# Optimization experiments

Hardware: AMD Instinct MI355X
Metric: run time of the kernel (lower is better)

The kernel has to match this reference:

```python
import jax, jax.numpy as jnp
import numpy as np

V_A, V_HP = 256, 256
H_A, H_HP = 2048, 4096
DEPTH = 12


def lstm_cell(x, h, c, W_ih, W_hh, b_ih, b_hh):
    # PyTorch LSTM cell: gate order i, f, g, o along the 4H axis.
    gates = x @ W_ih.T + h @ W_hh.T + (b_ih + b_hh)
    i, f, g, o = jnp.split(gates, 4, axis=-1)
    c_new = jax.nn.sigmoid(f) * c + jax.nn.sigmoid(i) * jnp.tanh(g)
    h_new = jax.nn.sigmoid(o) * jnp.tanh(c_new)
    return h_new, c_new


def setup_inputs() -> dict:
    key = jax.random.key(0)
    ks = jax.random.split(key, 16)
    s = jnp.float32(0.02)
    f32 = jnp.float32
    return {
        "x_thought_vec_arch": jax.random.normal(ks[0], (1, 1, H_A), f32),
        "x_thought_vec_arch_hp": jax.random.normal(ks[1], (1, 1, H_HP), f32),
        # arch LSTM (input V_A, hidden H_A)
        "W_ih_a": jax.random.normal(ks[2], (4 * H_A, V_A), f32) * s,
        "W_hh_a": jax.random.normal(ks[3], (4 * H_A, H_A), f32) * s,
        "b_ih_a": jax.random.normal(ks[4], (4 * H_A,), f32) * s,
        "b_hh_a": jax.random.normal(ks[5], (4 * H_A,), f32) * s,
        # arch_out Linear (H_A -> V_A)
        "W_out_a": jax.random.normal(ks[6], (V_A, H_A), f32) * s,
        "b_out_a": jax.random.normal(ks[7], (V_A,), f32) * s,
        # hp_summarizer Linear (H_HP -> H_HP//2)
        "W_sum": jax.random.normal(ks[8], (H_HP // 2, H_HP), f32) * s,
        "b_sum": jax.random.normal(ks[9], (H_HP // 2,), f32) * s,
        # arch_hp LSTM (input V_A + V_HP, hidden H_HP)
        "W_ih_hp": jax.random.normal(ks[10], (4 * H_HP, V_A + V_HP), f32) * s,
        "W_hh_hp": jax.random.normal(ks[11], (4 * H_HP, H_HP), f32) * s,
        "b_ih_hp": jax.random.normal(ks[12], (4 * H_HP,), f32) * s,
        "b_hh_hp": jax.random.normal(ks[13], (4 * H_HP,), f32) * s,
        # arch_hp_out Linear (H_HP -> V_HP)
        "W_out_hp": jax.random.normal(ks[14], (V_HP, H_HP), f32) * s,
        "b_out_hp": jax.random.normal(ks[15], (V_HP,), f32) * s,
    }


def reference(x_thought_vec_arch, x_thought_vec_arch_hp,
              W_ih_a, W_hh_a, b_ih_a, b_hh_a, W_out_a, b_out_a,
              W_sum, b_sum, W_ih_hp, W_hh_hp, b_ih_hp, b_hh_hp,
              W_out_hp, b_out_hp):
    h_a, h_hp = x_thought_vec_arch, x_thought_vec_arch_hp  # thought vecs used as hidden states
    c_a = jnp.zeros_like(h_a)
    c_hp = jnp.zeros_like(h_hp)
    a = jnp.full((1, 1, V_A), 1.0 / V_A, jnp.float32)       # SOS soft one-hot
    a_hp = jnp.full((1, 1, V_HP), 1.0 / V_HP, jnp.float32)

    def step(carry, _):
        a, a_hp, h_a, c_a, h_hp, c_hp = carry
        # forward_arch: seq_len=1 so LSTM output == new hidden
        h_a, c_a = lstm_cell(a, h_a, c_a, W_ih_a, W_hh_a, b_ih_a, b_hh_a)
        a = jax.nn.softmax(h_a @ W_out_a.T + b_out_a, axis=-1)
        # forward_arch_hp (keeps the original's swapped hx=(c_hp, prev_h_hp)):
        h_sum = jax.nn.relu(h_hp @ W_sum.T + b_sum)
        prev_h_hp = jnp.concatenate([h_a, h_sum], axis=-1)   # used as CELL state
        inp = jnp.concatenate([a, a_hp], axis=-1)
        h_hp, c_hp = lstm_cell(inp, c_hp, prev_h_hp, W_ih_hp, W_hh_hp, b_ih_hp, b_hh_hp)
        a_hp = jax.nn.softmax(h_hp @ W_out_hp.T + b_out_hp, axis=-1)
        return (a, a_hp, h_a, c_a, h_hp, c_hp), (a, a_hp)

    _, (ys_a, ys_hp) = jax.lax.scan(step, (a, a_hp, h_a, c_a, h_hp, c_hp), None, length=DEPTH)
    # torch.cat(list_of_(1,1,V), dim=1) -> (1, DEPTH, V)
    arch = ys_a.reshape(DEPTH, V_A)[None]
    arch_hp = ys_hp.reshape(DEPTH, V_HP)[None]
    return arch, arch_hp
```

## Files before the change

### kernel.cpp

```cpp
#include <hip/hip_runtime.h>
#include <hip/hip_fp16.h>
#include <hip/hip_cooperative_groups.h>

namespace cg = cooperative_groups;

#define H_A   2048
#define H_HP  4096
#define DEPTH 12

struct Half8 { __half2 a, b, c, d; };
struct Half4 { __half2 a, b; };

__device__ __forceinline__ float fsig_(float x) { return 1.0f / (1.0f + __expf(-x)); }
__device__ __forceinline__ float ftanh_(float x) {
    return 1.0f - 2.0f / (__expf(2.0f * x) + 1.0f);
}
__device__ __forceinline__ float dot4_(float4 a, float4 b) {
    return a.x * b.x + a.y * b.y + a.z * b.z + a.w * b.w;
}
__device__ __forceinline__ float dot8h_(Half8 w, float4 x0, float4 x1) {
    float2 wa = __half22float2(w.a), wb = __half22float2(w.b);
    float2 wc = __half22float2(w.c), wd = __half22float2(w.d);
    return wa.x * x0.x + wa.y * x0.y + wb.x * x0.z + wb.y * x0.w +
           wc.x * x1.x + wc.y * x1.y + wd.x * x1.z + wd.y * x1.w;
// ... 25 lines not shown
        a2 += __shfl_xor(a2, off, 64);
        a3 += __shfl_xor(a3, off, 64);
    }
}

struct Params {
    const float *x_a, *x_hp;
    const float *W_ih_a, *W_hh_a, *b_ih_a, *b_hh_a;
    const float *W_out_a, *b_out_a, *W_sum, *b_sum;
    const float *W_ih_hp, *W_hh_hp, *b_ih_hp, *b_hh_hp, *W_out_hp, *b_out_hp;
    __half *hW_ih_a, *hW_hh_a, *hW_sum, *hW_ih_hp, *hW_hh_hp, *hW_out_a, *hW_out_hp;
    float *gates_a, *h_sum, *gacc, *h_a, *c_a0, *c_a1, *h_hp, *c_hp;
    float *logits_a, *logits_hp, *a_vec, *out;
};

__global__ __launch_bounds__(256) void decoder_persistent(Params p)
{
    cg::grid_group grid = cg::this_grid();
    __shared__ float sbuf[2056];
    const int tid = threadIdx.x, lane = tid & 63, wv = tid >> 6;
    const int waveId = (blockIdx.x << 2) | wv;
    const int nw = (gridDim.x << 2);

    for (int t = 0; t < DEPTH; ++t) {
        {
            const int limit = (t == 0) ? 26624 : 26880;
            for (int r = waveId; r < limit; r += nw) {
                if (r < 8192) {
                    float acc;
                    if (t == 0) {
                        float4 wf = ((const float4*)(p.W_ih_a + (size_t)r * 256))[lane];
                        ((Half4*)(p.hW_ih_a + (size_t)r * 256))[lane] = cvt4_(wf);
                        acc = (wf.x + wf.y + wf.z + wf.w) * (1.0f / 256.0f);
                        const float4* whf = (const float4*)(p.W_hh_a + (size_t)r * H_A);
                        const float4* xh = (const float4*)p.x_a;
                        Half4* dsth = (Half4*)(p.hW_hh_a + (size_t)r * H_A);
#pragma unroll
                        for (int it = 0; it < 8; ++it) {
                            int idx = it * 64 + lane;
                            float4 w = whf[idx];
                            dsth[idx] = cvt4_(w);
                            acc += dot4_(w, xh[idx]);
                        }
                    } else {
                        Half4 w = ((const Half4*)(p.hW_ih_a + (size_t)r * 256))[lane];
                        float4 x = ((const float4*)p.a_vec)[lane];
                        float2 w0 = __half22float2(w.a), w1 = __half22float2(w.b);
                        acc = w0.x * x.x + w0.y * x.y + w1.x * x.z + w1.y * x.w;
                        const Half8* wh = (const Half8*)(p.hW_hh_a + (size_t)r * H_A);
                        const float4* xh = (const float4*)p.h_a;
#pragma unroll
                        for (int it = 0; it < 4; ++it) {
                            int idx = it * 64 + lane;
                            acc += dot8h_(wh[idx], xh[2 * idx], xh[2 * idx + 1]);
                        }
                    }
                    acc = waveReduceSum(acc);
                    if (lane == 0) p.gates_a[r] = acc + p.b_ih_a[r] + p.b_hh_a[r];
                } else if (r < 10240) {
                    const int rr = r - 8192;
                    float acc = 0.0f;
                    if (t == 0) {
                        const float4* wf = (const float4*)(p.W_sum + (size_t)rr * H_HP);
                        const float4* xx = (const float4*)p.x_hp;
                        Half4* dsth = (Half4*)(p.hW_sum + (size_t)rr * H_HP);
#pragma unroll
                        for (int it = 0; it < 16; ++it) {
                            int idx = it * 64 + lane;
                            float4 w = wf[idx];
                            dsth[idx] = cvt4_(w);
                            acc += dot4_(w, xx[idx]);
                        }
                    } else {
                        const Half8* ww = (const Half8*)(p.hW_sum + (size_t)rr * H_HP);
                        const float4* xx = (const float4*)p.h_hp;
#pragma unroll
                        for (int it = 0; it < 8; ++it) {
                            int idx = it * 64 + lane;
                            acc += dot8h_(ww[idx], xx[2 * idx], xx[2 * idx + 1]);
                        }
                    }
                    acc = waveReduceSum(acc);
                    if (lane == 0) p.h_sum[rr] = fmaxf(acc + p.b_sum[rr], 0.0f);
                } else if (r < 26624) {
                    const int rg = r - 10240;
                    if (t == 0) {
                        const float4* wf = (const float4*)(p.W_hh_hp + (size_t)rg * H_HP);
                        Half4* dsth = (Half4*)(p.hW_hh_hp + (size_t)rg * H_HP);
#pragma unroll
                        for (int it = 0; it < 16; ++it) {
                            int idx = it * 64 + lane;
                            dsth[idx] = cvt4_(wf[idx]);
                        }
                        if (lane == 0) p.gacc[rg] = p.b_ih_hp[rg] + p.b_hh_hp[rg];
                    } else {
                        const Half8* ww = (const Half8*)(p.hW_hh_hp + (size_t)rg * H_HP);
                        const float4* xx = (const float4*)p.c_hp;
                        float acc = 0.0f;
#pragma unroll
                        for (int it = 0; it < 8; ++it) {
                            int idx = it * 64 + lane;
                            acc += dot8h_(ww[idx], xx[2 * idx], xx[2 * idx + 1]);
                        }
                        acc = waveReduceSum(acc);
                        if (lane == 0) p.gacc[rg] = acc + p.b_ih_hp[rg] + p.b_hh_hp[rg];
                    }
                } else {
                    const int ro = r - 26624;
                    float acc = 0.0f;
                    const float4* xx = (const float4*)p.h_hp;
                    if (t == 1) {
                        const float4* wf = (const float4*)(p.W_out_hp + (size_t)ro * H_HP);
                        Half4* dsth = (Half4*)(p.hW_out_hp + (size_t)ro * H_HP);
#pragma unroll
                        for (int it = 0; it < 16; ++it) {
                            int idx = it * 64 + lane;
                            float4 w = wf[idx];
                            dsth[idx] = cvt4_(w);
                            acc += dot4_(w, xx[idx]);
                        }
                    } else {
                        const Half8* ww = (const Half8*)(p.hW_out_hp + (size_t)ro * H_HP);
#pragma unroll
                        for (int it = 0; it < 8; ++it) {
                            int idx = it * 64 + lane;
                            acc += dot8h_(ww[idx], xx[2 * idx], xx[2 * idx + 1]);
                        }
                    }
                    acc = waveReduceSum(acc);
                    if (lane == 0) p.logits_hp[ro] = acc + p.b_out_hp[ro];
                }
            }
        }
        grid.sync();

        if (blockIdx.x < 16) {
            float* h_s = sbuf;
            const float* cin = (t & 1) ? p.c_a1 : p.c_a0;
            float* cout = (t & 1) ? p.c_a0 : p.c_a1;
#pragma unroll
            for (int k = 0; k < 8; ++k) {
                int e = tid + k * 256;
                float gi = p.gates_a[e], gf = p.gates_a[H_A + e];
                float gg = p.gates_a[2 * H_A + e], go = p.gates_a[3 * H_A + e];
                float ci = (t == 0) ? 0.0f : cin[e];
                float c = fsig_(gf) * ci + fsig_(gi) * ftanh_(gg);
                float h = fsig_(go) * ftanh_(c);
                h_s[e] = h;
                if (blockIdx.x == 0) { cout[e] = c; p.h_a[e] = h; }
            }
            __syncthreads();
            const float4* h4 = (const float4*)h_s;
            int row = (blockIdx.x << 4) | (wv << 2);
            for (int j = 0; j < 4; ++j, ++row) {
                float acc = 0.0f;
                if (t == 0) {
                    const float4* wf = (const float4*)(p.W_out_a + (size_t)row * H_A);
                    Half4* dsth = (Half4*)(p.hW_out_a + (size_t)row * H_A);
#pragma unroll
                    for (int it = 0; it < 8; ++it) {
                        int idx = it * 64 + lane;
                        float4 w = wf[idx];
                        dsth[idx] = cvt4_(w);
                        acc += dot4_(w, h4[idx]);
                    }
                } else {
                    const Half8* ww = (const Half8*)(p.hW_out_a + (size_t)row * H_A);
#pragma unroll
                    for (int it = 0; it < 4; ++it) {
                        int idx = it * 64 + lane;
                        acc += dot8h_(ww[idx], h4[2 * idx], h4[2 * idx + 1]);
                    }
                }
                acc = waveReduceSum(acc);
                if (lane == 0) p.logits_a[row] = acc + p.b_out_a[row];
            }
        }
        grid.sync();

        {
            float* p_all = sbuf;
            float* red   = sbuf + 512;
            float la = p.logits_a[tid];
            float lh = (t == 0) ? 0.0f : p.logits_hp[tid];
            float ma = la, mh = lh;
#pragma unroll
            for (int off = 32; off > 0; off >>= 1) {
                ma = fmaxf(ma, __shfl_xor(ma, off, 64));
                mh = fmaxf(mh, __shfl_xor(mh, off, 64));
            }
            if (lane == 0) { red[wv] = ma; red[4 + wv] = mh; }
            __syncthreads();
            ma = fmaxf(fmaxf(red[0], red[1]), fmaxf(red[2], red[3]));
            mh = fmaxf(fmaxf(red[4], red[5]), fmaxf(red[6], red[7]));
            __syncthreads();
            float ea = __expf(la - ma), eh = __expf(lh - mh);
            float sa = waveReduceSum(ea), sh = waveReduceSum(eh);
            if (lane == 0) { red[wv] = sa; red[4 + wv] = sh; }
            __syncthreads();
            sa = red[0] + red[1] + red[2] + red[3];
            sh = red[4] + red[5] + red[6] + red[7];
            float pa = ea / sa, ph = eh / sh;
            p_all[tid] = pa;
            p_all[256 + tid] = ph;
            if (blockIdx.x == 0) {
                p.a_vec[tid] = pa;
                p.out[(size_t)t * 256 + tid] = pa;
                if (t > 0) p.out[3072 + (size_t)(t - 1) * 256 + tid] = ph;
            }
            __syncthreads();
            float4 xa = ((const float4*)p_all)[2 * lane];
            float4 xb = ((const float4*)p_all)[2 * lane + 1];
            for (int e = waveId; e < H_HP; e += nw) {
                float s0, s1, s2, s3;
                if (t == 0) {
                    auto rowdot_cvt = [&](int r) -> float {
                        const float4* wf = (const float4*)(p.W_ih_hp + (size_t)r * 512);
                        float4 u = wf[2 * lane], v = wf[2 * lane + 1];
                        ((Half8*)(p.hW_ih_hp + (size_t)r * 512))[lane] = cvt8_(u, v);
                        return dot4_(u, xa) + dot4_(v, xb);
                    };
                    s0 = rowdot_cvt(e);
                    s1 = rowdot_cvt(4096 + e);
                    s2 = rowdot_cvt(8192 + e);
                    s3 = rowdot_cvt(12288 + e);
                } else {
                    Half8 w0 = ((const Half8*)(p.hW_ih_hp + (size_t)e * 512))[lane];
                    Half8 w1 = ((const Half8*)(p.hW_ih_hp + (size_t)(4096 + e) * 512))[lane];
                    Half8 w2 = ((const Half8*)(p.hW_ih_hp + (size_t)(8192 + e) * 512))[lane];
                    Half8 w3 = ((const Half8*)(p.hW_ih_hp + (size_t)(12288 + e) * 512))[lane];
                    s0 = dot8h_(w0, xa, xb);
                    s1 = dot8h_(w1, xa, xb);
                    s2 = dot8h_(w2, xa, xb);
                    s3 = dot8h_(w3, xa, xb);
                }
                waveReduce4(s0, s1, s2, s3);
                if (lane == 0) {
                    float gi = s0 + p.gacc[e];
                    float gf = s1 + p.gacc[4096 + e];
                    float gg = s2 + p.gacc[8192 + e];
                    float go = s3 + p.gacc[12288 + e];
                    float prev = (e < H_A) ? p.h_a[e] : p.h_sum[e - H_A];
                    float c = fsig_(gf) * prev + fsig_(gi) * ftanh_(gg);
                    float h = fsig_(go) * ftanh_(c);
                    p.c_hp[e] = c;
                    p.h_hp[e] = h;
                }
            }
        }
        grid.sync();
    }

    if (blockIdx.x < 16) {
        int row = (blockIdx.x << 4) | (wv << 2);
        const float4* xx = (const float4*)p.h_hp;
        for (int j = 0; j < 4; ++j, ++row) {
            const Half8* ww = (const Half8*)(p.hW_out_hp + (size_t)row * H_HP);
            float acc = 0.0f;
#pragma unroll
            for (int it = 0; it < 8; ++it) {
                int idx = it * 64 + lane;
                acc += dot8h_(ww[idx], xx[2 * idx], xx[2 * idx + 1]);
            }
            acc = waveReduceSum(acc);
            if (lane == 0) p.logits_hp[row] = acc + p.b_out_hp[row];
        }
    }
    grid.sync();
    if (blockIdx.x == 0) {
        float* red = sbuf + 512;
        float v = p.logits_hp[tid];
        float m = v;
#pragma unroll
        for (int off = 32; off > 0; off >>= 1) m = fmaxf(m, __shfl_xor(m, off, 64));
        if (lane == 0) red[wv] = m;
        __syncthreads();
        m = fmaxf(fmaxf(red[0], red[1]), fmaxf(red[2], red[3]));
        __syncthreads();
        float e = __expf(v - m);
        float s = waveReduceSum(e);
        if (lane == 0) red[wv] = s;
        __syncthreads();
        s = red[0] + red[1] + red[2] + red[3];
        p.out[3072 + 11 * 256 + tid] = e / s;
    }
}

__global__ void k_init(const float* __restrict__ x_a, const float* __restrict__ x_hp,
                       float* __restrict__ h_a, float* __restrict__ c_a0,
                       float* __restrict__ h_hp, float* __restrict__ c_hp,
                       float* __restrict__ a_vec, float* __restrict__ logits_hp)
{
    int i = blockIdx.x * 256 + threadIdx.x;
    if (i < H_A)  { h_a[i] = x_a[i];  c_a0[i] = 0.0f; }
    if (i < H_HP) { h_hp[i] = x_hp[i]; c_hp[i] = 0.0f; }
    if (i < 256)  { a_vec[i] = 1.0f / 256.0f; logits_hp[i] = 0.0f; }
}

__global__ __launch_bounds__(256) void k_f2h_batched(
    const float* __restrict__ W_ih_a,  __half* __restrict__ hW_ih_a,
    const float* __restrict__ W_hh_a,  __half* __restrict__ hW_hh_a,
    const float* __restrict__ W_sum,   __half* __restrict__ hW_sum,
    const float* __restrict__ W_ih_hp, __half* __restrict__ hW_ih_hp,
    const float* __restrict__ W_out_a, __half* __restrict__ hW_out_a,
    const float* __restrict__ W_out_hp,__half* __restrict__ hW_out_hp)
{
    int i = blockIdx.x * 256 + threadIdx.x;
    const float* src; __half* dst; int base;
    if      (i < 262144)  { src = W_ih_a;   dst = hW_ih_a;   base = 0; }
    else if (i < 2359296) { src = W_hh_a;   dst = hW_hh_a;   base = 262144; }
    else if (i < 3407872) { src = W_sum;    dst = hW_sum;    base = 2359296; }
    else if (i < 4456448) { src = W_ih_hp;  dst = hW_ih_hp;  base = 3407872; }
    else if (i < 4521984) { src = W_out_a;  dst = hW_out_a;  base = 4456448; }
    else if (i < 4653056) { src = W_out_hp; dst = hW_out_hp; base = 4521984; }
    else return;
    int j = i - base;
    float4 a = ((const float4*)src)[2 * j];
    float4 b = ((const float4*)src)[2 * j + 1];
    ((Half8*)dst)[j] = cvt8_(a, b);
}

__global__ __launch_bounds__(256) void kA_fused_gemv(
    const __half* __restrict__ hW_ih_a, const __half* __restrict__ hW_hh_a,
    const float* __restrict__ b_ih_a, const float* __restrict__ b_hh_a,
    const __half* __restrict__ hW_sum,  const float* __restrict__ b_sum,
    __half* __restrict__ hW_hh_hp, const float* __restrict__ W_hh_hp_f32,
    const float* __restrict__ b_ih_hp, const float* __restrict__ b_hh_hp,
    const float* __restrict__ a_vec,  const float* __restrict__ h_a,
    const float* __restrict__ h_hp,   const float* __restrict__ c_hp,
    float* __restrict__ gates_a, float* __restrict__ h_sum_o,
    float* __restrict__ gacc_hp, int step0)
{
    const int lane = threadIdx.x & 63;
    const int wave = (blockIdx.x << 2) | (threadIdx.x >> 6);

    if (wave < 8192) {
        const int r = wave;
        const __half2* wp = (const __half2*)(hW_ih_a + (size_t)r * 256);
        __half2 w0h = wp[2 * lane], w1h = wp[2 * lane + 1];
        float4 x = ((const float4*)a_vec)[lane];
        float2 w0 = __half22float2(w0h), w1 = __half22float2(w1h);
        float acc = w0.x * x.x + w0.y * x.y + w1.x * x.z + w1.y * x.w;
        const Half8* wh = (const Half8*)(hW_hh_a + (size_t)r * H_A);
        const float4* xh = (const float4*)h_a;
#pragma unroll
        for (int it = 0; it < 4; ++it) {
            int idx = it * 64 + lane;
            acc += dot8h_(wh[idx], xh[2 * idx], xh[2 * idx + 1]);
        }
        acc = waveReduceSum(acc);
        if (lane == 0) gates_a[r] = acc + b_ih_a[r] + b_hh_a[r];
    } else if (wave < 10240) {
        const int r = wave - 8192;
        const Half8* ww = (const Half8*)(hW_sum + (size_t)r * H_HP);
        const float4* xx = (const float4*)h_hp;
        float acc = 0.0f;
#pragma unroll
        for (int it = 0; it < 8; ++it) {
            int idx = it * 64 + lane;
            acc += dot8h_(ww[idx], xx[2 * idx], xx[2 * idx + 1]);
        }
        acc = waveReduceSum(acc);
        if (lane == 0) h_sum_o[r] = fmaxf(acc + b_sum[r], 0.0f);
    } else {
        const int r = wave - 10240;
        if (step0) {
            const float4* src = (const float4*)(W_hh_hp_f32 + (size_t)r * H_HP);
            Half8* dst = (Half8*)(hW_hh_hp + (size_t)r * H_HP);
#pragma unroll
            for (int it = 0; it < 8; ++it) {
                int idx = it * 64 + lane;
                dst[idx] = cvt8_(src[2 * idx], src[2 * idx + 1]);
            }
            if (lane == 0) gacc_hp[r] = b_ih_hp[r] + b_hh_hp[r];
        } else {
            const Half8* ww = (const Half8*)(hW_hh_hp + (size_t)r * H_HP);
            const float4* xx = (const float4*)c_hp;
            float acc = 0.0f;
#pragma unroll
            for (int it = 0; it < 8; ++it) {
                int idx = it * 64 + lane;
                acc += dot8h_(ww[idx], xx[2 * idx], xx[2 * idx + 1]);
            }
            acc = waveReduceSum(acc);
            if (lane == 0) gacc_hp[r] = acc + b_ih_hp[r] + b_hh_hp[r];
        }
    }
}

__global__ __launch_bounds__(256) void kB_arch(
    const float* __restrict__ gates_a, const float* __restrict__ c_in,
    float* __restrict__ c_out, float* __restrict__ h_a_g,
    const __half* __restrict__ hW_out_a, const float* __restrict__ b_out_a,
    float* __restrict__ logits_a)
{
    __shared__ float h_s[H_A];
    const int t = threadIdx.x;
#pragma unroll
    for (int k = 0; k < 8; ++k) {
        int e = t + k * 256;
        float gi = gates_a[e];
        float gf = gates_a[H_A + e];
        float gg = gates_a[2 * H_A + e];
        float go = gates_a[3 * H_A + e];
        float c_new = fsig_(gf) * c_in[e] + fsig_(gi) * ftanh_(gg);
        float h = fsig_(go) * ftanh_(c_new);
        h_s[e] = h;
        if (blockIdx.x == 0) { c_out[e] = c_new; h_a_g[e] = h; }
    }
    __syncthreads();
    const int lane = t & 63;
    const int r = (blockIdx.x << 2) | (t >> 6);
    const Half8* w8 = (const Half8*)(hW_out_a + (size_t)r * H_A);
    const float4* h4 = (const float4*)h_s;
    float acc = 0.0f;
#pragma unroll
    for (int it = 0; it < 4; ++it) {
        int idx = it * 64 + lane;
        acc += dot8h_(w8[idx], h4[2 * idx], h4[2 * idx + 1]);
    }
    acc = waveReduceSum(acc);
    if (lane == 0) logits_a[r] = acc + b_out_a[r];
}

__global__ __launch_bounds__(256) void kC_softmax_ih(
    const float* __restrict__ logits_a, const float* __restrict__ logits_hp,
    const __half* __restrict__ hW_ih_hp, float* __restrict__ gacc_hp,
    float* __restrict__ a_vec_g, float* __restrict__ out_a,
    float* __restrict__ out_hp)
{
    __shared__ float p_all[512];
    __shared__ float red[8];
    const int t = threadIdx.x, lane = t & 63, wv = t >> 6;
    float la = logits_a[t], lh = logits_hp[t];
    float ma = la, mh = lh;
#pragma unroll
    for (int off = 32; off > 0; off >>= 1) {
        ma = fmaxf(ma, __shfl_xor(ma, off, 64));
        mh = fmaxf(mh, __shfl_xor(mh, off, 64));
    }
    if (lane == 0) { red[wv] = ma; red[4 + wv] = mh; }
    __syncthreads();
    ma = fmaxf(fmaxf(red[0], red[1]), fmaxf(red[2], red[3]));
    mh = fmaxf(fmaxf(red[4], red[5]), fmaxf(red[6], red[7]));
    __syncthreads();
    float ea = __expf(la - ma), eh = __expf(lh - mh);
    float sa = waveReduceSum(ea), sh = waveReduceSum(eh);
    if (lane == 0) { red[wv] = sa; red[4 + wv] = sh; }
    __syncthreads();
    sa = red[0] + red[1] + red[2] + red[3];
    sh = red[4] + red[5] + red[6] + red[7];
    float pa = ea / sa, ph = eh / sh;
    p_all[t] = pa;
    p_all[256 + t] = ph;
    if (blockIdx.x == 0) {
        a_vec_g[t] = pa;
        out_a[t] = pa;
        out_hp[t] = ph;
    }
    __syncthreads();
    const float4* x4 = (const float4*)p_all;
    float4 xa = x4[2 * lane], xb = x4[2 * lane + 1];
    const int gw = (blockIdx.x << 2) | wv;
#pragma unroll
    for (int rr = 0; rr < 4; ++rr) {
        int r = (gw << 2) | rr;
        Half8 w = ((const Half8*)(hW_ih_hp + (size_t)r * 512))[lane];
        float acc = dot8h_(w, xa, xb);
        acc = waveReduceSum(acc);
        if (lane == 0) gacc_hp[r] += acc;
    }
}

__global__ __launch_bounds__(256) void kD_hp(
    const float* __restrict__ gacc_hp, const float* __restrict__ h_a,
    const float* __restrict__ h_sum, float* __restrict__ c_hp_g,
    float* __restrict__ h_hp_g,
    const __half* __restrict__ hW_out_hp, const float* __restrict__ b_out_hp,
    float* __restrict__ logits_hp)
{
    __shared__ float h_s[H_HP];
    const int t = threadIdx.x;
#pragma unroll
    for (int k = 0; k < 16; ++k) {
        int e = t + k * 256;
        float gi = gacc_hp[e];
        float gf = gacc_hp[H_HP + e];
        float gg = gacc_hp[2 * H_HP + e];
        float go = gacc_hp[3 * H_HP + e];
        float prev = (e < H_A) ? h_a[e] : h_sum[e - H_A];
        float c = fsig_(gf) * prev + fsig_(gi) * ftanh_(gg);
        float h = fsig_(go) * ftanh_(c);
        h_s[e] = h;
        if (blockIdx.x == 0) { c_hp_g[e] = c; h_hp_g[e] = h; }
    }
    __syncthreads();
    const int lane = t & 63;
    const int r = (blockIdx.x << 2) | (t >> 6);
    const Half8* w8 = (const Half8*)(hW_out_hp + (size_t)r * H_HP);
    const float4* x4 = (const float4*)h_s;
    float acc = 0.0f;
#pragma unroll
    for (int it = 0; it < 8; ++it) {
        int idx = it * 64 + lane;
        acc += dot8h_(w8[idx], x4[2 * idx], x4[2 * idx + 1]);
    }
    acc = waveReduceSum(acc);
    if (lane == 0) logits_hp[r] = acc + b_out_hp[r];
}

__global__ __launch_bounds__(256) void k_softmax_tail(
    const float* __restrict__ logits_hp, float* __restrict__ outp)
{
    __shared__ float red[4];
    const int t = threadIdx.x, lane = t & 63, wv = t >> 6;
    float v = logits_hp[t];
    float m = v;
#pragma unroll
    for (int off = 32; off > 0; off >>= 1) m = fmaxf(m, __shfl_xor(m, off, 64));
    if (lane == 0) red[wv] = m;
    __syncthreads();
    m = fmaxf(fmaxf(red[0], red[1]), fmaxf(red[2], red[3]));
    __syncthreads();
    float e = __expf(v - m);
    float s = waveReduceSum(e);
    if (lane == 0) red[wv] = s;
    __syncthreads();
    s = red[0] + red[1] + red[2] + red[3];
    outp[t] = e / s;
}


extern "C" void kernel_launch(void* const* d_in, const int* in_sizes, int n_in,
                              void* d_out, int out_size, void* d_ws, size_t ws_size,
                              hipStream_t stream)
{
    Params p;
    p.x_a      = (const float*)d_in[0];
    p.x_hp     = (const float*)d_in[1];
    p.W_ih_a   = (const float*)d_in[2];
    p.W_hh_a   = (const float*)d_in[3];
    p.b_ih_a   = (const float*)d_in[4];
    p.b_hh_a   = (const float*)d_in[5];
    p.W_out_a  = (const float*)d_in[6];
// ... 15 lines not shown
    p.hW_out_a  = p.hW_hh_hp  + 67108864;
    p.hW_out_hp = p.hW_out_a  + 524288;
    float* ws = (float*)(p.hW_out_hp + 1048576);

    p.gates_a   = ws;
    p.h_sum     = ws + 8192;
    p.gacc      = ws + 10240;
    p.h_a       = ws + 26624;
    p.c_a0      = ws + 28672;
    p.c_a1      = ws + 30720;
    p.h_hp      = ws + 32768;
    p.c_hp      = ws + 36864;
    p.logits_a  = ws + 40960;
    p.logits_hp = ws + 41216;
    p.a_vec     = ws + 41472;
    float* dummy = ws + 41728;
    p.out       = (float*)d_out;

    int blocksPerCU = 0;
    hipError_t qerr = hipOccupancyMaxActiveBlocksPerMultiprocessor(
        &blocksPerCU, (const void*)decoder_persistent, 256, 0);
    if (qerr == hipSuccess && blocksPerCU >= 1) {
        int grid = blocksPerCU * 256;
        if (grid > 1024) grid = 1024;
        void* kargs[] = { (void*)&p };
        hipError_t lerr = hipLaunchCooperativeKernel(
            (const void*)decoder_persistent, dim3(grid), dim3(256), kargs, 0, stream);
        if (lerr == hipSuccess) return;
    }

    k_init<<<16, 256, 0, stream>>>(p.x_a, p.x_hp, p.h_a, p.c_a0, p.h_hp, p.c_hp,
                                   p.a_vec, p.logits_hp);
    k_f2h_batched<<<18176, 256, 0, stream>>>(
        p.W_ih_a, p.hW_ih_a, p.W_hh_a, p.hW_hh_a, p.W_sum, p.hW_sum,
        p.W_ih_hp, p.hW_ih_hp, p.W_out_a, p.hW_out_a, p.W_out_hp, p.hW_out_hp);

    float* c_a[2] = { p.c_a0, p.c_a1 };
    float* out = p.out;
    for (int t = 0; t < DEPTH; ++t) {
        kA_fused_gemv<<<6656, 256, 0, stream>>>(
            p.hW_ih_a, p.hW_hh_a, p.b_ih_a, p.b_hh_a, p.hW_sum, p.b_sum,
            p.hW_hh_hp, p.W_hh_hp, p.b_ih_hp, p.b_hh_hp,
            p.a_vec, p.h_a, p.h_hp, p.c_hp,
            p.gates_a, p.h_sum, p.gacc, (t == 0) ? 1 : 0);

        kB_arch<<<64, 256, 0, stream>>>(p.gates_a, c_a[t & 1], c_a[(t + 1) & 1],
                                        p.h_a, p.hW_out_a, p.b_out_a, p.logits_a);

        kC_softmax_ih<<<1024, 256, 0, stream>>>(
            p.logits_a, p.logits_hp, p.hW_ih_hp, p.gacc,
            p.a_vec, out + (size_t)t * 256,
            (t == 0) ? dummy : out + 3072 + (size_t)(t - 1) * 256);

        kD_hp<<<64, 256, 0, stream>>>(p.gacc, p.h_a, p.h_sum, p.c_hp, p.h_hp,
                                      p.hW_out_hp, p.b_out_hp, p.logits_hp);
    }

    k_softmax_tail<<<1, 256, 0, stream>>>(p.logits_hp, out + 3072 + 11 * 256);
}
```

Measured before the change: 1.140 ms.

## Replace cooperative persistent kernel with per-step multi-kernel launches

Removes the cooperative persistent kernel and its grid-wide syncs, and drives each decode step with three ordinary launches (kA, kB, kC) plus two tail kernels. The fp16 weight conversion stays fused into the step-0 and step-1 GEMV passes, and the output-projection GEMV for the hp branch is folded into the next step's kA. The goal is to replace costly grid barriers with kernel boundaries and to use full-occupancy grids instead of a capped persistent grid. In exchange it pays about 38 launch overheads.

```diff
diff --git a/kernel.cpp b/kernel.cpp
--- a/kernel.cpp
+++ b/kernel.cpp
@@ -1,8 +1,5 @@
 #include <hip/hip_runtime.h>
 #include <hip/hip_fp16.h>
-#include <hip/hip_cooperative_groups.h>
-
-namespace cg = cooperative_groups;
 
 #define H_A   2048
 #define H_HP  4096
@@ -63,425 +60,170 @@
     float *logits_a, *logits_hp, *a_vec, *out;
 };
 
-__global__ __launch_bounds__(256) void decoder_persistent(Params p)
-{
-    cg::grid_group grid = cg::this_grid();
-    __shared__ float sbuf[2056];
-    const int tid = threadIdx.x, lane = tid & 63, wv = tid >> 6;
-    const int waveId = (blockIdx.x << 2) | wv;
-    const int nw = (gridDim.x << 2);
-
-    for (int t = 0; t < DEPTH; ++t) {
-        {
-            const int limit = (t == 0) ? 26624 : 26880;
-            for (int r = waveId; r < limit; r += nw) {
-                if (r < 8192) {
-                    float acc;
-                    if (t == 0) {
-                        float4 wf = ((const float4*)(p.W_ih_a + (size_t)r * 256))[lane];
-                        ((Half4*)(p.hW_ih_a + (size_t)r * 256))[lane] = cvt4_(wf);
-                        acc = (wf.x + wf.y + wf.z + wf.w) * (1.0f / 256.0f);
-                        const float4* whf = (const float4*)(p.W_hh_a + (size_t)r * H_A);
-                        const float4* xh = (const float4*)p.x_a;
-                        Half4* dsth = (Half4*)(p.hW_hh_a + (size_t)r * H_A);
-#pragma unroll
-                        for (int it = 0; it < 8; ++it) {
-                            int idx = it * 64 + lane;
-                            float4 w = whf[idx];
-                            dsth[idx] = cvt4_(w);
-                            acc += dot4_(w, xh[idx]);
-                        }
-                    } else {
-                        Half4 w = ((const Half4*)(p.hW_ih_a + (size_t)r * 256))[lane];
-                        float4 x = ((const float4*)p.a_vec)[lane];
-                        float2 w0 = __half22float2(w.a), w1 = __half22float2(w.b);
-                        acc = w0.x * x.x + w0.y * x.y + w1.x * x.z + w1.y * x.w;
-                        const Half8* wh = (const Half8*)(p.hW_hh_a + (size_t)r * H_A);
-                        const float4* xh = (const float4*)p.h_a;
-#pragma unroll
-                        for (int it = 0; it < 4; ++it) {
-                            int idx = it * 64 + lane;
-                            acc += dot8h_(wh[idx], xh[2 * idx], xh[2 * idx + 1]);
-                        }
-                    }
-                    acc = waveReduceSum(acc);
-                    if (lane == 0) p.gates_a[r] = acc + p.b_ih_a[r] + p.b_hh_a[r];
-                } else if (r < 10240) {
-                    const int rr = r - 8192;
-                    float acc = 0.0f;
-                    if (t == 0) {
-                        const float4* wf = (const float4*)(p.W_sum + (size_t)rr * H_HP);
-                        const float4* xx = (const float4*)p.x_hp;
-                        Half4* dsth = (Half4*)(p.hW_sum + (size_t)rr * H_HP);
-#pragma unroll
-                        for (int it = 0; it < 16; ++it) {
-                            int idx = it * 64 + lane;
-                            float4 w = wf[idx];
-                            dsth[idx] = cvt4_(w);
-                            acc += dot4_(w, xx[idx]);
-                        }
-                    } else {
-                        const Half8* ww = (const Half8*)(p.hW_sum + (size_t)rr * H_HP);
-                        const float4* xx = (const float4*)p.h_hp;
-#pragma unroll
-                        for (int it = 0; it < 8; ++it) {
-                            int idx = it * 64 + lane;
-                            acc += dot8h_(ww[idx], xx[2 * idx], xx[2 * idx + 1]);
-                        }
-                    }
-                    acc = waveReduceSum(acc);
-                    if (lane == 0) p.h_sum[rr] = fmaxf(acc + p.b_sum[rr], 0.0f);
-                } else if (r < 26624) {
-                    const int rg = r - 10240;
-                    if (t == 0) {
-                        const float4* wf = (const float4*)(p.W_hh_hp + (size_t)rg * H_HP);
-                        Half4* dsth = (Half4*)(p.hW_hh_hp + (size_t)rg * H_HP);
-#pragma unroll
-                        for (int it = 0; it < 16; ++it) {
-                            int idx = it * 64 + lane;
-                            dsth[idx] = cvt4_(wf[idx]);
-                        }
-                        if (lane == 0) p.gacc[rg] = p.b_ih_hp[rg] + p.b_hh_hp[rg];
-                    } else {
-                        const Half8* ww = (const Half8*)(p.hW_hh_hp + (size_t)rg * H_HP);
-                        const float4* xx = (const float4*)p.c_hp;
-                        float acc = 0.0f;
-#pragma unroll
-                        for (int it = 0; it < 8; ++it) {
-                            int idx = it * 64 + lane;
-                            acc += dot8h_(ww[idx], xx[2 * idx], xx[2 * idx + 1]);
-                        }
-                        acc = waveReduceSum(acc);
-                        if (lane == 0) p.gacc[rg] = acc + p.b_ih_hp[rg] + p.b_hh_hp[rg];
-                    }
-                } else {
-                    const int ro = r - 26624;
-                    float acc = 0.0f;
-                    const float4* xx = (const float4*)p.h_hp;
-                    if (t == 1) {
-                        const float4* wf = (const float4*)(p.W_out_hp + (size_t)ro * H_HP);
-                        Half4* dsth = (Half4*)(p.hW_out_hp + (size_t)ro * H_HP);
-#pragma unroll
-                        for (int it = 0; it < 16; ++it) {
-                            int idx = it * 64 + lane;
-                            float4 w = wf[idx];
-                            dsth[idx] = cvt4_(w);
-                            acc += dot4_(w, xx[idx]);
-                        }
-                    } else {
-                        const Half8* ww = (const Half8*)(p.hW_out_hp + (size_t)ro * H_HP);
-#pragma unroll
-                        for (int it = 0; it < 8; ++it) {
-                            int idx = it * 64 + lane;
-                            acc += dot8h_(ww[idx], xx[2 * idx], xx[2 * idx + 1]);
-                        }
-                    }
-                    acc = waveReduceSum(acc);
-                    if (lane == 0) p.logits_hp[ro] = acc + p.b_out_hp[ro];
-                }
-            }
-        }
-        grid.sync();
-
-        if (blockIdx.x < 16) {
-            float* h_s = sbuf;
-            const float* cin = (t & 1) ? p.c_a1 : p.c_a0;
-            float* cout = (t & 1) ? p.c_a0 : p.c_a1;
-#pragma unroll
-            for (int k = 0; k < 8; ++k) {
-                int e = tid + k * 256;
-                float gi = p.gates_a[e], gf = p.gates_a[H_A + e];
-                float gg = p.gates_a[2 * H_A + e], go = p.gates_a[3 * H_A + e];
-                float ci = (t == 0) ? 0.0f : cin[e];
-                float c = fsig_(gf) * ci + fsig_(gi) * ftanh_(gg);
-                float h = fsig_(go) * ftanh_(c);
-                h_s[e] = h;
-                if (blockIdx.x == 0) { cout[e] = c; p.h_a[e] = h; }
-            }
-            __syncthreads();
-            const float4* h4 = (const float4*)h_s;
-            int row = (blockIdx.x << 4) | (wv << 2);
-            for (int j = 0; j < 4; ++j, ++row) {
-                float acc = 0.0f;
-                if (t == 0) {
-                    const float4* wf = (const float4*)(p.W_out_a + (size_t)row * H_A);
-                    Half4* dsth = (Half4*)(p.hW_out_a + (size_t)row * H_A);
-#pragma unroll
-                    for (int it = 0; it < 8; ++it) {
-                        int idx = it * 64 + lane;
-                        float4 w = wf[idx];
-                        dsth[idx] = cvt4_(w);
-                        acc += dot4_(w, h4[idx]);
-                    }
-                } else {
-                    const Half8* ww = (const Half8*)(p.hW_out_a + (size_t)row * H_A);
-#pragma unroll
-                    for (int it = 0; it < 4; ++it) {
-                        int idx = it * 64 + lane;
-                        acc += dot8h_(ww[idx], h4[2 * idx], h4[2 * idx + 1]);
-                    }
-                }
-                acc = waveReduceSum(acc);
-                if (lane == 0) p.logits_a[row] = acc + p.b_out_a[row];
-            }
-        }
-        grid.sync();
-
-        {
-            float* p_all = sbuf;
-            float* red   = sbuf + 512;
-            float la = p.logits_a[tid];
-            float lh = (t == 0) ? 0.0f : p.logits_hp[tid];
-            float ma = la, mh = lh;
-#pragma unroll
-            for (int off = 32; off > 0; off >>= 1) {
-                ma = fmaxf(ma, __shfl_xor(ma, off, 64));
-                mh = fmaxf(mh, __shfl_xor(mh, off, 64));
-            }
-            if (lane == 0) { red[wv] = ma; red[4 + wv] = mh; }
-            __syncthreads();
-            ma = fmaxf(fmaxf(red[0], red[1]), fmaxf(red[2], red[3]));
-            mh = fmaxf(fmaxf(red[4], red[5]), fmaxf(red[6], red[7]));
-            __syncthreads();
-            float ea = __expf(la - ma), eh = __expf(lh - mh);
-            float sa = waveReduceSum(ea), sh = waveReduceSum(eh);
-            if (lane == 0) { red[wv] = sa; red[4 + wv] = sh; }
-            __syncthreads();
-            sa = red[0] + red[1] + red[2] + red[3];
-            sh = red[4] + red[5] + red[6] + red[7];
-            float pa = ea / sa, ph = eh / sh;
-            p_all[tid] = pa;
-            p_all[256 + tid] = ph;
-            if (blockIdx.x == 0) {
-                p.a_vec[tid] = pa;
-                p.out[(size_t)t * 256 + tid] = pa;
-                if (t > 0) p.out[3072 + (size_t)(t - 1) * 256 + tid] = ph;
-            }
-            __syncthreads();
-            float4 xa = ((const float4*)p_all)[2 * lane];
-            float4 xb = ((const float4*)p_all)[2 * lane + 1];
-            for (int e = waveId; e < H_HP; e += nw) {
-                float s0, s1, s2, s3;
-                if (t == 0) {
-                    auto rowdot_cvt = [&](int r) -> float {
-                        const float4* wf = (const float4*)(p.W_ih_hp + (size_t)r * 512);
-                        float4 u = wf[2 * lane], v = wf[2 * lane + 1];
-                        ((Half8*)(p.hW_ih_hp + (size_t)r * 512))[lane] = cvt8_(u, v);
-                        return dot4_(u, xa) + dot4_(v, xb);
-                    };
-                    s0 = rowdot_cvt(e);
-                    s1 = rowdot_cvt(4096 + e);
-                    s2 = rowdot_cvt(8192 + e);
-                    s3 = rowdot_cvt(12288 + e);
-                } else {
-                    Half8 w0 = ((const Half8*)(p.hW_ih_hp + (size_t)e * 512))[lane];
-                    Half8 w1 = ((const Half8*)(p.hW_ih_hp + (size_t)(4096 + e) * 512))[lane];
-                    Half8 w2 = ((const Half8*)(p.hW_ih_hp + (size_t)(8192 + e) * 512))[lane];
-                    Half8 w3 = ((const Half8*)(p.hW_ih_hp + (size_t)(12288 + e) * 512))[lane];
-                    s0 = dot8h_(w0, xa, xb);
-                    s1 = dot8h_(w1, xa, xb);
-                    s2 = dot8h_(w2, xa, xb);
-                    s3 = dot8h_(w3, xa, xb);
-                }
-                waveReduce4(s0, s1, s2, s3);
-                if (lane == 0) {
-                    float gi = s0 + p.gacc[e];
-                    float gf = s1 + p.gacc[4096 + e];
-                    float gg = s2 + p.gacc[8192 + e];
-                    float go = s3 + p.gacc[12288 + e];
-                    float prev = (e < H_A) ? p.h_a[e] : p.h_sum[e - H_A];
-                    float c = fsig_(gf) * prev + fsig_(gi) * ftanh_(gg);
-                    float h = fsig_(go) * ftanh_(c);
-                    p.c_hp[e] = c;
-                    p.h_hp[e] = h;
-                }
-            }
-        }
-        grid.sync();
-    }
-
-    if (blockIdx.x < 16) {
-        int row = (blockIdx.x << 4) | (wv << 2);
-        const float4* xx = (const float4*)p.h_hp;
-        for (int j = 0; j < 4; ++j, ++row) {
-            const Half8* ww = (const Half8*)(p.hW_out_hp + (size_t)row * H_HP);
-            float acc = 0.0f;
-#pragma unroll
-            for (int it = 0; it < 8; ++it) {
-                int idx = it * 64 + lane;
-                acc += dot8h_(ww[idx], xx[2 * idx], xx[2 * idx + 1]);
-            }
-            acc = waveReduceSum(acc);
-            if (lane == 0) p.logits_hp[row] = acc + p.b_out_hp[row];
-        }
-    }
-    grid.sync();
-    if (blockIdx.x == 0) {
-        float* red = sbuf + 512;
-        float v = p.logits_hp[tid];
-        float m = v;
-#pragma unroll
-        for (int off = 32; off > 0; off >>= 1) m = fmaxf(m, __shfl_xor(m, off, 64));
-        if (lane == 0) red[wv] = m;
-        __syncthreads();
-        m = fmaxf(fmaxf(red[0], red[1]), fmaxf(red[2], red[3]));
-        __syncthreads();
-        float e = __expf(v - m);
-        float s = waveReduceSum(e);
-        if (lane == 0) red[wv] = s;
-        __syncthreads();
-        s = red[0] + red[1] + red[2] + red[3];
-        p.out[3072 + 11 * 256 + tid] = e / s;
-    }
-}
-
-__global__ void k_init(const float* __restrict__ x_a, const float* __restrict__ x_hp,
-                       float* __restrict__ h_a, float* __restrict__ c_a0,
-                       float* __restrict__ h_hp, float* __restrict__ c_hp,
-                       float* __restrict__ a_vec, float* __restrict__ logits_hp)
-{
-    int i = blockIdx.x * 256 + threadIdx.x;
-    if (i < H_A)  { h_a[i] = x_a[i];  c_a0[i] = 0.0f; }
-    if (i < H_HP) { h_hp[i] = x_hp[i]; c_hp[i] = 0.0f; }
-    if (i < 256)  { a_vec[i] = 1.0f / 256.0f; logits_hp[i] = 0.0f; }
-}
-
-__global__ __launch_bounds__(256) void k_f2h_batched(
-    const float* __restrict__ W_ih_a,  __half* __restrict__ hW_ih_a,
-    const float* __restrict__ W_hh_a,  __half* __restrict__ hW_hh_a,
-    const float* __restrict__ W_sum,   __half* __restrict__ hW_sum,
-    const float* __restrict__ W_ih_hp, __half* __restrict__ hW_ih_hp,
-    const float* __restrict__ W_out_a, __half* __restrict__ hW_out_a,
-    const float* __restrict__ W_out_hp,__half* __restrict__ hW_out_hp)
-{
-    int i = blockIdx.x * 256 + threadIdx.x;
-    const float* src; __half* dst; int base;
-    if      (i < 262144)  { src = W_ih_a;   dst = hW_ih_a;   base = 0; }
-    else if (i < 2359296) { src = W_hh_a;   dst = hW_hh_a;   base = 262144; }
-    else if (i < 3407872) { src = W_sum;    dst = hW_sum;    base = 2359296; }
-    else if (i < 4456448) { src = W_ih_hp;  dst = hW_ih_hp;  base = 3407872; }
-    else if (i < 4521984) { src = W_out_a;  dst = hW_out_a;  base = 4456448; }
-    else if (i < 4653056) { src = W_out_hp; dst = hW_out_hp; base = 4521984; }
-    else return;
-    int j = i - base;
-    float4 a = ((const float4*)src)[2 * j];
-    float4 b = ((const float4*)src)[2 * j + 1];
-    ((Half8*)dst)[j] = cvt8_(a, b);
-}
-
-__global__ __launch_bounds__(256) void kA_fused_gemv(
-    const __half* __restrict__ hW_ih_a, const __half* __restrict__ hW_hh_a,
-    const float* __restrict__ b_ih_a, const float* __restrict__ b_hh_a,
-    const __half* __restrict__ hW_sum,  const float* __restrict__ b_sum,
-    __half* __restrict__ hW_hh_hp, const float* __restrict__ W_hh_hp_f32,
-    const float* __restrict__ b_ih_hp, const float* __restrict__ b_hh_hp,
-    const float* __restrict__ a_vec,  const float* __restrict__ h_a,
-    const float* __restrict__ h_hp,   const float* __restrict__ c_hp,
-    float* __restrict__ gates_a, float* __restrict__ h_sum_o,
-    float* __restrict__ gacc_hp, int step0)
+__global__ __launch_bounds__(256) void kA(Params p, int t)
 {
     const int lane = threadIdx.x & 63;
     const int wave = (blockIdx.x << 2) | (threadIdx.x >> 6);
 
     if (wave < 8192) {
         const int r = wave;
-        const __half2* wp = (const __half2*)(hW_ih_a + (size_t)r * 256);
-        __half2 w0h = wp[2 * lane], w1h = wp[2 * lane + 1];
-        float4 x = ((const float4*)a_vec)[lane];
-        float2 w0 = __half22float2(w0h), w1 = __half22float2(w1h);
-        float acc = w0.x * x.x + w0.y * x.y + w1.x * x.z + w1.y * x.w;
-        const Half8* wh = (const Half8*)(hW_hh_a + (size_t)r * H_A);
-        const float4* xh = (const float4*)h_a;
+        float acc;
+        if (t == 0) {
+            float4 wf = ((const float4*)(p.W_ih_a + (size_t)r * 256))[lane];
+            ((Half4*)(p.hW_ih_a + (size_t)r * 256))[lane] = cvt4_(wf);
+            acc = (wf.x + wf.y + wf.z + wf.w) * (1.0f / 256.0f);
+            const float4* whf = (const float4*)(p.W_hh_a + (size_t)r * H_A);
+            const float4* xh = (const float4*)p.x_a;
+            Half4* dsth = (Half4*)(p.hW_hh_a + (size_t)r * H_A);
+#pragma unroll
+            for (int it = 0; it < 8; ++it) {
+                int idx = it * 64 + lane;
+                float4 w = whf[idx];
+                dsth[idx] = cvt4_(w);
+                acc += dot4_(w, xh[idx]);
+            }
+        } else {
+            Half4 w = ((const Half4*)(p.hW_ih_a + (size_t)r * 256))[lane];
+            float4 x = ((const float4*)p.a_vec)[lane];
+            float2 w0 = __half22float2(w.a), w1 = __half22float2(w.b);
+            acc = w0.x * x.x + w0.y * x.y + w1.x * x.z + w1.y * x.w;
+            const Half8* wh = (const Half8*)(p.hW_hh_a + (size_t)r * H_A);
+            const float4* xh = (const float4*)p.h_a;
+#pragma unroll
+            for (int it = 0; it < 4; ++it) {
+                int idx = it * 64 + lane;
+                acc += dot8h_(wh[idx], xh[2 * idx], xh[2 * idx + 1]);
+            }
+        }
+        acc = waveReduceSum(acc);
+        if (lane == 0) p.gates_a[r] = acc + p.b_ih_a[r] + p.b_hh_a[r];
+    } else if (wave < 10240) {
+        const int rr = wave - 8192;
+        float acc = 0.0f;
+        if (t == 0) {
+            const float4* wf = (const float4*)(p.W_sum + (size_t)rr * H_HP);
+            const float4* xx = (const float4*)p.x_hp;
+            Half4* dsth = (Half4*)(p.hW_sum + (size_t)rr * H_HP);
+#pragma unroll
+            for (int it = 0; it < 16; ++it) {
+                int idx = it * 64 + lane;
+                float4 w = wf[idx];
+                dsth[idx] = cvt4_(w);
+                acc += dot4_(w, xx[idx]);
+            }
+        } else {
+            const Half8* ww = (const Half8*)(p.hW_sum + (size_t)rr * H_HP);
+            const float4* xx = (const float4*)p.h_hp;
+#pragma unroll
+            for (int it = 0; it < 8; ++it) {
+                int idx = it * 64 + lane;
+                acc += dot8h_(ww[idx], xx[2 * idx], xx[2 * idx + 1]);
+            }
+        }
+        acc = waveReduceSum(acc);
+        if (lane == 0) p.h_sum[rr] = fmaxf(acc + p.b_sum[rr], 0.0f);
+    } else if (wave < 26624) {
+        const int rg = wave - 10240;
+        if (t == 0) {
+            const float4* wf = (const float4*)(p.W_hh_hp + (size_t)rg * H_HP);
+            Half4* dsth = (Half4*)(p.hW_hh_hp + (size_t)rg * H_HP);
+#pragma unroll
+            for (int it = 0; it < 16; ++it) {
+                int idx = it * 64 + lane;
+                dsth[idx] = cvt4_(wf[idx]);
+            }
+            if (lane == 0) p.gacc[rg] = p.b_ih_hp[rg] + p.b_hh_hp[rg];
+        } else {
+            const Half8* ww = (const Half8*)(p.hW_hh_hp + (size_t)rg * H_HP);
+            const float4* xx = (const float4*)p.c_hp;
+            float acc = 0.0f;
+#pragma unroll
+            for (int it = 0; it < 8; ++it) {
+                int idx = it * 64 + lane;
+                acc += dot8h_(ww[idx], xx[2 * idx], xx[2 * idx + 1]);
+            }
+            acc = waveReduceSum(acc);
+            if (lane == 0) p.gacc[rg] = acc + p.b_ih_hp[rg] + p.b_hh_hp[rg];
+        }
+    } else {
+        if (t == 0) return;
+        const int ro = wave - 26624;
+        float acc = 0.0f;
+        const float4* xx = (const float4*)p.h_hp;
+        if (t == 1) {
+            const float4* wf = (const float4*)(p.W_out_hp + (size_t)ro * H_HP);
+            Half4* dsth = (Half4*)(p.hW_out_hp + (size_t)ro * H_HP);
+#pragma unroll
+            for (int it = 0; it < 16; ++it) {
+                int idx = it * 64 + lane;
+                float4 w = wf[idx];
+                dsth[idx] = cvt4_(w);
+                acc += dot4_(w, xx[idx]);
+            }
+        } else {
+            const Half8* ww = (const Half8*)(p.hW_out_hp + (size_t)ro * H_HP);
+#pragma unroll
+            for (int it = 0; it < 8; ++it) {
+                int idx = it * 64 + lane;
+                acc += dot8h_(ww[idx], xx[2 * idx], xx[2 * idx + 1]);
+            }
+        }
+        acc = waveReduceSum(acc);
+        if (lane == 0) p.logits_hp[ro] = acc + p.b_out_hp[ro];
+    }
+}
+
+__global__ __launch_bounds__(256) void kB(Params p, int t)
+{
+    __shared__ float h_s[H_A];
+    const int tid = threadIdx.x;
+    const float* cin = (t & 1) ? p.c_a1 : p.c_a0;
+    float* cout = (t & 1) ? p.c_a0 : p.c_a1;
+#pragma unroll
+    for (int k = 0; k < 8; ++k) {
+        int e = tid + k * 256;
+        float gi = p.gates_a[e], gf = p.gates_a[H_A + e];
+        float gg = p.gates_a[2 * H_A + e], go = p.gates_a[3 * H_A + e];
+        float ci = (t == 0) ? 0.0f : cin[e];
+        float c = fsig_(gf) * ci + fsig_(gi) * ftanh_(gg);
+        float h = fsig_(go) * ftanh_(c);
+        h_s[e] = h;
+        if (blockIdx.x == 0) { cout[e] = c; p.h_a[e] = h; }
+    }
+    __syncthreads();
+    const int lane = tid & 63;
+    const int r = (blockIdx.x << 2) | (tid >> 6);
+    const float4* h4 = (const float4*)h_s;
+    float acc = 0.0f;
+    if (t == 0) {
+        const float4* wf = (const float4*)(p.W_out_a + (size_t)r * H_A);
+        Half4* dsth = (Half4*)(p.hW_out_a + (size_t)r * H_A);
+#pragma unroll
+        for (int it = 0; it < 8; ++it) {
+            int idx = it * 64 + lane;
+            float4 w = wf[idx];
+            dsth[idx] = cvt4_(w);
+            acc += dot4_(w, h4[idx]);
+        }
+    } else {
+        const Half8* ww = (const Half8*)(p.hW_out_a + (size_t)r * H_A);
 #pragma unroll
         for (int it = 0; it < 4; ++it) {
             int idx = it * 64 + lane;
-            acc += dot8h_(wh[idx], xh[2 * idx], xh[2 * idx + 1]);
-        }
-        acc = waveReduceSum(acc);
-        if (lane == 0) gates_a[r] = acc + b_ih_a[r] + b_hh_a[r];
-    } else if (wave < 10240) {
-        const int r = wave - 8192;
-        const Half8* ww = (const Half8*)(hW_sum + (size_t)r * H_HP);
-        const float4* xx = (const float4*)h_hp;
-        float acc = 0.0f;
-#pragma unroll
-        for (int it = 0; it < 8; ++it) {
-            int idx = it * 64 + lane;
-            acc += dot8h_(ww[idx], xx[2 * idx], xx[2 * idx + 1]);
-        }
-        acc = waveReduceSum(acc);
-        if (lane == 0) h_sum_o[r] = fmaxf(acc + b_sum[r], 0.0f);
-    } else {
-        const int r = wave - 10240;
-        if (step0) {
-            const float4* src = (const float4*)(W_hh_hp_f32 + (size_t)r * H_HP);
-            Half8* dst = (Half8*)(hW_hh_hp + (size_t)r * H_HP);
-#pragma unroll
-            for (int it = 0; it < 8; ++it) {
-                int idx = it * 64 + lane;
-                dst[idx] = cvt8_(src[2 * idx], src[2 * idx + 1]);
-            }
-            if (lane == 0) gacc_hp[r] = b_ih_hp[r] + b_hh_hp[r];
-        } else {
-            const Half8* ww = (const Half8*)(hW_hh_hp + (size_t)r * H_HP);
-            const float4* xx = (const float4*)c_hp;
-            float acc = 0.0f;
-#pragma unroll
-            for (int it = 0; it < 8; ++it) {
-                int idx = it * 64 + lane;
-                acc += dot8h_(ww[idx], xx[2 * idx], xx[2 * idx + 1]);
-            }
-            acc = waveReduceSum(acc);
-            if (lane == 0) gacc_hp[r] = acc + b_ih_hp[r] + b_hh_hp[r];
-        }
-    }
-}
-
-__global__ __launch_bounds__(256) void kB_arch(
-    const float* __restrict__ gates_a, const float* __restrict__ c_in,
-    float* __restrict__ c_out, float* __restrict__ h_a_g,
-    const __half* __restrict__ hW_out_a, const float* __restrict__ b_out_a,
-    float* __restrict__ logits_a)
-{
-    __shared__ float h_s[H_A];
-    const int t = threadIdx.x;
-#pragma unroll
-    for (int k = 0; k < 8; ++k) {
-        int e = t + k * 256;
-        float gi = gates_a[e];
-        float gf = gates_a[H_A + e];
-        float gg = gates_a[2 * H_A + e];
-        float go = gates_a[3 * H_A + e];
-        float c_new = fsig_(gf) * c_in[e] + fsig_(gi) * ftanh_(gg);
-        float h = fsig_(go) * ftanh_(c_new);
-        h_s[e] = h;
-        if (blockIdx.x == 0) { c_out[e] = c_new; h_a_g[e] = h; }
-    }
-    __syncthreads();
-    const int lane = t & 63;
-    const int r = (blockIdx.x << 2) | (t >> 6);
-    const Half8* w8 = (const Half8*)(hW_out_a + (size_t)r * H_A);
-    const float4* h4 = (const float4*)h_s;
-    float acc = 0.0f;
-#pragma unroll
-    for (int it = 0; it < 4; ++it) {
-        int idx = it * 64 + lane;
-        acc += dot8h_(w8[idx], h4[2 * idx], h4[2 * idx + 1]);
+            acc += dot8h_(ww[idx], h4[2 * idx], h4[2 * idx + 1]);
+        }
     }
     acc = waveReduceSum(acc);
-    if (lane == 0) logits_a[r] = acc + b_out_a[r];
-}
-
-__global__ __launch_bounds__(256) void kC_softmax_ih(
-    const float* __restrict__ logits_a, const float* __restrict__ logits_hp,
-    const __half* __restrict__ hW_ih_hp, float* __restrict__ gacc_hp,
-    float* __restrict__ a_vec_g, float* __restrict__ out_a,
-    float* __restrict__ out_hp)
+    if (lane == 0) p.logits_a[r] = acc + p.b_out_a[r];
+}
+
+__global__ __launch_bounds__(256) void kC(Params p, int t)
 {
     __shared__ float p_all[512];
     __shared__ float red[8];
-    const int t = threadIdx.x, lane = t & 63, wv = t >> 6;
-    float la = logits_a[t], lh = logits_hp[t];
+    const int tid = threadIdx.x, lane = tid & 63, wv = tid >> 6;
+    float la = p.logits_a[tid];
+    float lh = (t == 0) ? 0.0f : p.logits_hp[tid];
     float ma = la, mh = lh;
 #pragma unroll
     for (int off = 32; off > 0; off >>= 1) {
@@ -500,70 +242,74 @@
     sa = red[0] + red[1] + red[2] + red[3];
     sh = red[4] + red[5] + red[6] + red[7];
     float pa = ea / sa, ph = eh / sh;
-    p_all[t] = pa;
-    p_all[256 + t] = ph;
+    p_all[tid] = pa;
+    p_all[256 + tid] = ph;
     if (blockIdx.x == 0) {
-        a_vec_g[t] = pa;
-        out_a[t] = pa;
-        out_hp[t] = ph;
-    }
-    __syncthreads();
-    const float4* x4 = (const float4*)p_all;
-    float4 xa = x4[2 * lane], xb = x4[2 * lane + 1];
-    const int gw = (blockIdx.x << 2) | wv;
-#pragma unroll
-    for (int rr = 0; rr < 4; ++rr) {
-        int r = (gw << 2) | rr;
-        Half8 w = ((const Half8*)(hW_ih_hp + (size_t)r * 512))[lane];
-        float acc = dot8h_(w, xa, xb);
-        acc = waveReduceSum(acc);
-        if (lane == 0) gacc_hp[r] += acc;
-    }
-}
-
-__global__ __launch_bounds__(256) void kD_hp(
-    const float* __restrict__ gacc_hp, const float* __restrict__ h_a,
-    const float* __restrict__ h_sum, float* __restrict__ c_hp_g,
-    float* __restrict__ h_hp_g,
-    const __half* __restrict__ hW_out_hp, const float* __restrict__ b_out_hp,
-    float* __restrict__ logits_hp)
-{
-    __shared__ float h_s[H_HP];
-    const int t = threadIdx.x;
-#pragma unroll
-    for (int k = 0; k < 16; ++k) {
-        int e = t + k * 256;
-        float gi = gacc_hp[e];
-        float gf = gacc_hp[H_HP + e];
-        float gg = gacc_hp[2 * H_HP + e];
-        float go = gacc_hp[3 * H_HP + e];
-        float prev = (e < H_A) ? h_a[e] : h_sum[e - H_A];
+        p.a_vec[tid] = pa;
+        p.out[(size_t)t * 256 + tid] = pa;
+        if (t > 0) p.out[3072 + (size_t)(t - 1) * 256 + tid] = ph;
+    }
+    __syncthreads();
+    float4 xa = ((const float4*)p_all)[2 * lane];
+    float4 xb = ((const float4*)p_all)[2 * lane + 1];
+    const int e = (blockIdx.x << 2) | wv;
+    float s0, s1, s2, s3;
+    if (t == 0) {
+        auto rowdot_cvt = [&](int r) -> float {
+            const float4* wf = (const float4*)(p.W_ih_hp + (size_t)r * 512);
+            float4 u = wf[2 * lane], v = wf[2 * lane + 1];
+            ((Half8*)(p.hW_ih_hp + (size_t)r * 512))[lane] = cvt8_(u, v);
+            return dot4_(u, xa) + dot4_(v, xb);
+        };
+        s0 = rowdot_cvt(e);
+        s1 = rowdot_cvt(4096 + e);
+        s2 = rowdot_cvt(8192 + e);
+        s3 = rowdot_cvt(12288 + e);
+    } else {
+        Half8 w0 = ((const Half8*)(p.hW_ih_hp + (size_t)e * 512))[lane];
+        Half8 w1 = ((const Half8*)(p.hW_ih_hp + (size_t)(4096 + e) * 512))[lane];
+        Half8 w2 = ((const Half8*)(p.hW_ih_hp + (size_t)(8192 + e) * 512))[lane];
+        Half8 w3 = ((const Half8*)(p.hW_ih_hp + (size_t)(12288 + e) * 512))[lane];
+        s0 = dot8h_(w0, xa, xb);
+        s1 = dot8h_(w1, xa, xb);
+        s2 = dot8h_(w2, xa, xb);
+        s3 = dot8h_(w3, xa, xb);
+    }
+    waveReduce4(s0, s1, s2, s3);
+    if (lane == 0) {
+        float gi = s0 + p.gacc[e];
+        float gf = s1 + p.gacc[4096 + e];
+        float gg = s2 + p.gacc[8192 + e];
+        float go = s3 + p.gacc[12288 + e];
+        float prev = (e < H_A) ? p.h_a[e] : p.h_sum[e - H_A];
         float c = fsig_(gf) * prev + fsig_(gi) * ftanh_(gg);
         float h = fsig_(go) * ftanh_(c);
-        h_s[e] = h;
-        if (blockIdx.x == 0) { c_hp_g[e] = c; h_hp_g[e] = h; }
-    }
-    __syncthreads();
-    const int lane = t & 63;
-    const int r = (blockIdx.x << 2) | (t >> 6);
-    const Half8* w8 = (const Half8*)(hW_out_hp + (size_t)r * H_HP);
-    const float4* x4 = (const float4*)h_s;
+        p.c_hp[e] = c;
+        p.h_hp[e] = h;
+    }
+}
+
+__global__ __launch_bounds__(256) void kTail_gemv(Params p)
+{
+    const int lane = threadIdx.x & 63;
+    const int r = (blockIdx.x << 2) | (threadIdx.x >> 6);
+    const Half8* ww = (const Half8*)(p.hW_out_hp + (size_t)r * H_HP);
+    const float4* xx = (const float4*)p.h_hp;
     float acc = 0.0f;
 #pragma unroll
     for (int it = 0; it < 8; ++it) {
         int idx = it * 64 + lane;
-        acc += dot8h_(w8[idx], x4[2 * idx], x4[2 * idx + 1]);
+        acc += dot8h_(ww[idx], xx[2 * idx], xx[2 * idx + 1]);
     }
     acc = waveReduceSum(acc);
-    if (lane == 0) logits_hp[r] = acc + b_out_hp[r];
-}
-
-__global__ __launch_bounds__(256) void k_softmax_tail(
-    const float* __restrict__ logits_hp, float* __restrict__ outp)
+    if (lane == 0) p.logits_hp[r] = acc + p.b_out_hp[r];
+}
+
+__global__ __launch_bounds__(256) void kTail_softmax(Params p)
 {
     __shared__ float red[4];
-    const int t = threadIdx.x, lane = t & 63, wv = t >> 6;
-    float v = logits_hp[t];
+    const int tid = threadIdx.x, lane = tid & 63, wv = tid >> 6;
+    float v = p.logits_hp[tid];
     float m = v;
 #pragma unroll
     for (int off = 32; off > 0; off >>= 1) m = fmaxf(m, __shfl_xor(m, off, 64));
@@ -576,7 +322,7 @@
     if (lane == 0) red[wv] = s;
     __syncthreads();
     s = red[0] + red[1] + red[2] + red[3];
-    outp[t] = e / s;
+    p.out[3072 + 11 * 256 + tid] = e / s;
 }
 
 
@@ -622,47 +368,13 @@
     p.logits_a  = ws + 40960;
     p.logits_hp = ws + 41216;
     p.a_vec     = ws + 41472;
-    float* dummy = ws + 41728;
     p.out       = (float*)d_out;
 
-    int blocksPerCU = 0;
-    hipError_t qerr = hipOccupancyMaxActiveBlocksPerMultiprocessor(
-        &blocksPerCU, (const void*)decoder_persistent, 256, 0);
-    if (qerr == hipSuccess && blocksPerCU >= 1) {
-        int grid = blocksPerCU * 256;
-        if (grid > 1024) grid = 1024;
-        void* kargs[] = { (void*)&p };
-        hipError_t lerr = hipLaunchCooperativeKernel(
-            (const void*)decoder_persistent, dim3(grid), dim3(256), kargs, 0, stream);
-        if (lerr == hipSuccess) return;
-    }
-
-    k_init<<<16, 256, 0, stream>>>(p.x_a, p.x_hp, p.h_a, p.c_a0, p.h_hp, p.c_hp,
-                                   p.a_vec, p.logits_hp);
-    k_f2h_batched<<<18176, 256, 0, stream>>>(
-        p.W_ih_a, p.hW_ih_a, p.W_hh_a, p.hW_hh_a, p.W_sum, p.hW_sum,
-        p.W_ih_hp, p.hW_ih_hp, p.W_out_a, p.hW_out_a, p.W_out_hp, p.hW_out_hp);
-
-    float* c_a[2] = { p.c_a0, p.c_a1 };
-    float* out = p.out;
     for (int t = 0; t < DEPTH; ++t) {
-        kA_fused_gemv<<<6656, 256, 0, stream>>>(
-            p.hW_ih_a, p.hW_hh_a, p.b_ih_a, p.b_hh_a, p.hW_sum, p.b_sum,
-            p.hW_hh_hp, p.W_hh_hp, p.b_ih_hp, p.b_hh_hp,
-            p.a_vec, p.h_a, p.h_hp, p.c_hp,
-            p.gates_a, p.h_sum, p.gacc, (t == 0) ? 1 : 0);
-
-        kB_arch<<<64, 256, 0, stream>>>(p.gates_a, c_a[t & 1], c_a[(t + 1) & 1],
-                                        p.h_a, p.hW_out_a, p.b_out_a, p.logits_a);
-
-        kC_softmax_ih<<<1024, 256, 0, stream>>>(
-            p.logits_a, p.logits_hp, p.hW_ih_hp, p.gacc,
-            p.a_vec, out + (size_t)t * 256,
-            (t == 0) ? dummy : out + 3072 + (size_t)(t - 1) * 256);
-
-        kD_hp<<<64, 256, 0, stream>>>(p.gacc, p.h_a, p.h_sum, p.c_hp, p.h_hp,
-                                      p.hW_out_hp, p.b_out_hp, p.logits_hp);
-    }
-
-    k_softmax_tail<<<1, 256, 0, stream>>>(p.logits_hp, out + 3072 + 11 * 256);
-}
+        kA<<<6720, 256, 0, stream>>>(p, t);
+        kB<<<64, 256, 0, stream>>>(p, t);
+        kC<<<1024, 256, 0, stream>>>(p, t);
+    }
+    kTail_gemv<<<64, 256, 0, stream>>>(p);
+    kTail_softmax<<<1, 256, 0, stream>>>(p);
+}
```

Result: faster. 982.6 us (-13.8%).
